# Kernel tuning notes

Hardware: AMD Instinct MI355X
Metric: run time of the kernel (lower is better)

The kernel has to match this reference:

```python
import jax, jax.numpy as jnp
import numpy as np

HEADS = 8
DK = 64            # key_size == size_per_head
NEIGHBORS = 3
KSIZE = 1 + 2 * NEIGHBORS  # 7 (rate=1)


def setup_inputs() -> dict:
    key = jax.random.key(0)
    k1, k2, k3, k4 = jax.random.split(key, 4)
    B, HW, S, D = 2, 64, 256, 512
    inputs = jax.random.normal(k1, (B, HW, S, D), dtype=jnp.float32)
    pos_bias = jax.random.normal(k2, (HEADS, S, KSIZE), dtype=jnp.float32)
    W_qkv = jax.random.normal(k3, (D, 3 * HEADS * DK), dtype=jnp.float32) * 0.02
    W_out = jax.random.normal(k4, (HEADS * DK, D), dtype=jnp.float32) * 0.02
    return {"inputs": inputs, "pos_bias": pos_bias, "W_qkv": W_qkv, "W_out": W_out}


def reference(inputs, pos_bias, W_qkv, W_out):
    B, HW, S, D = inputs.shape
    # qkv projection (no bias), split into q, k, v
    qkv = inputs @ W_qkv                                   # [B,HW,S,3*H*DK]
    q, k, v = jnp.split(qkv, 3, axis=-1)
    q = (q / jnp.sqrt(jnp.float32(DK))).reshape(B, HW, S, HEADS, DK)
    k = k.reshape(B, HW, S, HEADS, DK)
    v = v.reshape(B, HW, S, HEADS, DK)

    # zero-pad keys/values along seq (faithful to F.pad with value=0)
    pad = NEIGHBORS
    kp = jnp.pad(k, ((0, 0), (0, 0), (pad, pad), (0, 0), (0, 0)))
    vp = jnp.pad(v, ((0, 0), (0, 0), (pad, pad), (0, 0), (0, 0)))

    # sliding-window gather: window w for query i covers padded positions i..i+KSIZE-1
    idx = jnp.arange(S)[:, None] + jnp.arange(KSIZE)[None, :]  # [S,KSIZE]
    kw = kp[:, :, idx]                                         # [B,HW,S,KSIZE,H,DK]
    vw = vp[:, :, idx]                                         # [B,HW,S,KSIZE,H,DK]

    # scores over the window
    attn = jnp.einsum('bnshd,bnswhd->bnswh', q, kw)            # [B,HW,S,KSIZE,H]
    # additive positional bias: [H,S,KSIZE] -> [S,KSIZE,H] broadcast
    attn = attn + jnp.transpose(pos_bias, (1, 2, 0))[None, None]
    attn = jax.nn.softmax(attn, axis=-2)                       # softmax over window dim

    out = jnp.einsum('bnswh,bnswhd->bnshd', attn, vw)          # [B,HW,S,H,DK]
    out = out.reshape(B, HW, S, HEADS * DK)
    return out @ W_out
```

## Files before the change

kernel.cpp:

```cpp
#include <hip/hip_runtime.h>
#include <hip/hip_bf16.h>
#include <cstdint>


typedef __bf16 bf16x8 __attribute__((ext_vector_type(8)));
typedef float f32x4 __attribute__((ext_vector_type(4)));

__device__ __forceinline__ uint16_t f2bf(float f) {
    uint32_t u = __builtin_bit_cast(uint32_t, f);
    return (uint16_t)((u + 0x7fffu + ((u >> 16) & 1u)) >> 16);
}
__device__ __forceinline__ float bflo(uint32_t u) { return __builtin_bit_cast(float, u << 16); }
__device__ __forceinline__ float bfhi(uint32_t u) { return __builtin_bit_cast(float, u & 0xffff0000u); }

__device__ __forceinline__ void unpack8(uint4 v, float* f) {
    f[0] = bflo(v.x); f[1] = bfhi(v.x);
    f[2] = bflo(v.y); f[3] = bfhi(v.y);
    f[4] = bflo(v.z); f[5] = bfhi(v.z);
    f[6] = bflo(v.w); f[7] = bfhi(v.w);
}
__device__ __forceinline__ uint32_t pack2(float a, float b) {
    return (uint32_t)f2bf(a) | ((uint32_t)f2bf(b) << 16);
}

#define GLOAD_LDS16(gp, lp)                                                        \
    __builtin_amdgcn_global_load_lds((const __attribute__((address_space(1))) void*)(gp), \
                                     (__attribute__((address_space(3))) void*)(lp), 16, 0, 0)

__global__ void cvt_f32_bf16(const float* __restrict__ in, uint16_t* __restrict__ out, int n8) {
    int i = blockIdx.x * 256 + threadIdx.x;
    if (i >= n8) return;
    const float4* p = (const float4*)in + (size_t)i * 2;
    float4 a = p[0], b = p[1];
    uint4 o;
    o.x = pack2(a.x, a.y);
    o.y = pack2(a.z, a.w);
    o.z = pack2(b.x, b.y);
    o.w = pack2(b.z, b.w);
    *((uint4*)out + i) = o;
}

__global__ void transpose_cvt(const float* __restrict__ in, uint16_t* __restrict__ out,
                              int R, int C) {
    int idx = blockIdx.x * 256 + threadIdx.x;
    if (idx >= R * C) return;
    int r = idx / C;
    int c = idx - r * C;
    out[(size_t)c * R + r] = f2bf(in[idx]);
}

__global__ void frag_shuffle(const uint16_t* __restrict__ BT, uint4* __restrict__ out,
                             int N, int K) {
    int idx = blockIdx.x * 256 + threadIdx.x;
    int kt_n = K / 32;
    int total = (N / 64) * kt_n * 4 * 64;
    if (idx >= total) return;
    int lane = idx & 63;
    int nt   = (idx >> 6) & 3;
    int kt   = (idx >> 8) % kt_n;
    int g    = (idx >> 8) / kt_n;
    int row  = g * 64 + nt * 16 + (lane & 15);
    int col4 = kt * 4 + (lane >> 4);
    out[idx] = ((const uint4*)BT)[(size_t)row * (K / 8) + col4];
}

template <bool F32OUT>
__global__ __launch_bounds__(256, 4)
void gemm_bt(const uint16_t* __restrict__ A, const uint4* __restrict__ Bfrag,
             void* __restrict__ Cout, int M, int N, int K) {
    __shared__ __align__(16) uint16_t As[128 * 32];

    const int tid  = threadIdx.x;
    const int lane = tid & 63;
    const int wv   = tid >> 6;
    const int r    = lane & 15;
    const int quad = lane >> 4;
    const int m_w  = (wv & 1) << 6;
    const int n_w  = (wv >> 1) << 6;
    const long bm0 = (long)blockIdx.x * 128;
    const long bn0 = (long)blockIdx.y * 128;
    const int KT   = K / 32;

    f32x4 acc[4][4];
#pragma unroll
    for (int i = 0; i < 4; ++i)
#pragma unroll
        for (int j = 0; j < 4; ++j) acc[i][j] = (f32x4){0.f, 0.f, 0.f, 0.f};

    const int c0 = tid, c1 = tid + 256;
    const uint16_t* pA0 = A + (bm0 + (c0 >> 2)) * (long)K + (c0 & 3) * 8;
    const uint16_t* pA1 = A + (bm0 + (c1 >> 2)) * (long)K + (c1 & 3) * 8;

    const int g = (int)((bn0 + n_w) >> 6);
    const uint4* pBf = Bfrag + ((size_t)g * KT * 4) * 64 + lane;

    for (int kt = 0; kt < KT; ++kt) {
        bf16x8 bfr[4];
#pragma unroll
        for (int nt = 0; nt < 4; ++nt)
            bfr[nt] = *(const bf16x8*)&pBf[(kt * 4 + nt) * 64];

        GLOAD_LDS16(pA0 + kt * 32, &As[c0 * 8]);
        GLOAD_LDS16(pA1 + kt * 32, &As[c1 * 8]);
        __syncthreads();

        bf16x8 af[4];
#pragma unroll
        for (int mt = 0; mt < 4; ++mt)
            af[mt] = *(const bf16x8*)&As[(m_w + mt * 16 + r) * 32 + quad * 8];
#pragma unroll
        for (int mt = 0; mt < 4; ++mt)
#pragma unroll
            for (int nt = 0; nt < 4; ++nt)
                acc[mt][nt] = __builtin_amdgcn_mfma_f32_16x16x32_bf16(af[mt], bfr[nt],
                                                                      acc[mt][nt], 0, 0, 0);
        __syncthreads();
    }

#pragma unroll
    for (int mt = 0; mt < 4; ++mt) {
#pragma unroll
        for (int i = 0; i < 4; ++i) {
            long m = bm0 + m_w + mt * 16 + quad * 4 + i;
            if (F32OUT) {
                float* crow = (float*)Cout + m * (long)N + bn0 + n_w + r;
#pragma unroll
                for (int nt = 0; nt < 4; ++nt) crow[nt * 16] = acc[mt][nt][i];
            } else {
                uint16_t* crow = (uint16_t*)Cout + m * (long)N + bn0 + n_w + r;
#pragma unroll
                for (int nt = 0; nt < 4; ++nt) crow[nt * 16] = f2bf(acc[mt][nt][i]);
            }
        }
    }
}

__global__ __launch_bounds__(256, 2)
void local_attn(const uint16_t* __restrict__ qkv, const float* __restrict__ pb,
                uint16_t* __restrict__ attn) {
    __shared__ uint4 smem[4096];

    const int h  = blockIdx.x & 7;
    const int bn = blockIdx.x >> 3;
    const int s  = threadIdx.x;
    const size_t base = (size_t)bn * 256 * 1536;

#pragma unroll
    for (int it = 0; it < 16; ++it) {
        int i   = threadIdx.x + it * 256;
        int a   = i >> 11;
        int idx = i & 2047;
        int sp  = idx >> 3;
        int c8  = idx & 7;
        const uint16_t* src = qkv + base + (size_t)sp * 1536 + 512 + a * 512 + h * 64 + c8 * 8;
        smem[a * 2048 + sp * 8 + (c8 ^ (sp & 7))] = *(const uint4*)src;
    }

    const uint16_t* qrow = qkv + base + (size_t)s * 1536 + h * 64;
    uint4 qc[8];
#pragma unroll
    for (int c = 0; c < 8; ++c) qc[c] = *(const uint4*)(qrow + c * 8);

    __syncthreads();

    float sc[7];
#pragma unroll
    for (int w = 0; w < 7; ++w) sc[w] = 0.f;

#pragma unroll
    for (int c = 0; c < 8; ++c) {
        float qf[8];
        unpack8(qc[c], qf);
#pragma unroll
        for (int w = 0; w < 7; ++w) {
            int sp = s + w - 3;
            if ((unsigned)sp < 256u) {
                uint4 kc = smem[sp * 8 + (c ^ (sp & 7))];
                float kf[8];
                unpack8(kc, kf);
#pragma unroll
                for (int j = 0; j < 8; ++j) sc[w] += qf[j] * kf[j];
            }
        }
    }

    const float* pbr = pb + ((size_t)h * 256 + s) * 7;
    float mx = -1e30f;
#pragma unroll
    for (int w = 0; w < 7; ++w) {
        sc[w] = sc[w] * 0.125f + pbr[w];
        mx = fmaxf(mx, sc[w]);
    }
    float p[7], sum = 0.f;
#pragma unroll
    for (int w = 0; w < 7; ++w) {
        p[w] = __expf(sc[w] - mx);
        sum += p[w];
    }
    const float inv = 1.f / sum;
#pragma unroll
    for (int w = 0; w < 7; ++w) p[w] *= inv;

    uint4 ov[8];
#pragma unroll
    for (int c = 0; c < 8; ++c) {
        float o[8] = {0.f, 0.f, 0.f, 0.f, 0.f, 0.f, 0.f, 0.f};
#pragma unroll
        for (int w = 0; w < 7; ++w) {
            int sp = s + w - 3;
            if ((unsigned)sp < 256u) {
                uint4 vc = smem[2048 + sp * 8 + (c ^ (sp & 7))];
                float vf[8];
                unpack8(vc, vf);
#pragma unroll
                for (int j = 0; j < 8; ++j) o[j] += p[w] * vf[j];
            }
        }
        ov[c].x = pack2(o[0], o[1]);
        ov[c].y = pack2(o[2], o[3]);
        ov[c].z = pack2(o[4], o[5]);
        ov[c].w = pack2(o[6], o[7]);
    }

    uint16_t* orow = attn + ((size_t)(bn * 256 + s)) * 512 + h * 64;
#pragma unroll
    for (int c = 0; c < 8; ++c) *(uint4*)(orow + c * 8) = ov[c];
}

extern "C" void kernel_launch(void* const* d_in, const int* in_sizes, int n_in,
                              void* d_out, int out_size, void* d_ws, size_t ws_size,
                              hipStream_t stream) {
    const float* X    = (const float*)d_in[0];
    const float* pb   = (const float*)d_in[1];
    const float* Wqkv = (const float*)d_in[2];
    const float* Wout = (const float*)d_in[3];
    float* out = (float*)d_out;

    char* ws = (char*)d_ws;
    uint16_t* WqkvT  = (uint16_t*)(ws);
    uint16_t* WoutT  = (uint16_t*)(ws + 1572864);
    uint4*    BfQkv  = (uint4*)(ws + 2097152);
    uint4*    BfOut  = (uint4*)(ws + 3670016);
    uint16_t* qkvb   = (uint16_t*)(ws + 4194304);
    uint16_t* Xb     = (uint16_t*)(ws + 104857600);
    uint16_t* attnb  = Xb;

    cvt_f32_bf16<<<(32768 * 512 / 8 + 255) / 256, 256, 0, stream>>>(X, Xb, 32768 * 512 / 8);
    transpose_cvt<<<(512 * 1536 + 255) / 256, 256, 0, stream>>>(Wqkv, WqkvT, 512, 1536);
    transpose_cvt<<<(512 * 512 + 255) / 256, 256, 0, stream>>>(Wout, WoutT, 512, 512);
    frag_shuffle<<<(1536 * 512 / 8 + 255) / 256, 256, 0, stream>>>(WqkvT, BfQkv, 1536, 512);
    frag_shuffle<<<(512 * 512 / 8 + 255) / 256, 256, 0, stream>>>(WoutT, BfOut, 512, 512);

    gemm_bt<false><<<dim3(256, 12), 256, 0, stream>>>(Xb, BfQkv, qkvb, 32768, 1536, 512);
    local_attn<<<1024, 256, 0, stream>>>(qkvb, pb, attnb);
    gemm_bt<true><<<dim3(256, 4), 256, 0, stream>>>(attnb, BfOut, out, 32768, 512, 512);
}
```

Measured before the change: 272.3 us.

## Load full-K A strip into LDS once and sweep all N tiles per block

```diff
diff --git a/kernel.cpp b/kernel.cpp
--- a/kernel.cpp
+++ b/kernel.cpp
@@ -27,17 +27,31 @@
     __builtin_amdgcn_global_load_lds((const __attribute__((address_space(1))) void*)(gp), \
                                      (__attribute__((address_space(3))) void*)(lp), 16, 0, 0)
 
-__global__ void cvt_f32_bf16(const float* __restrict__ in, uint16_t* __restrict__ out, int n8) {
-    int i = blockIdx.x * 256 + threadIdx.x;
-    if (i >= n8) return;
-    const float4* p = (const float4*)in + (size_t)i * 2;
-    float4 a = p[0], b = p[1];
-    uint4 o;
-    o.x = pack2(a.x, a.y);
-    o.y = pack2(a.z, a.w);
-    o.z = pack2(b.x, b.y);
-    o.w = pack2(b.z, b.w);
-    *((uint4*)out + i) = o;
+__global__ __launch_bounds__(256)
+void cvt_shuffle(const float* __restrict__ X, uint4* __restrict__ Afrag) {
+    __shared__ uint4 lds[4096];
+    const int g64 = blockIdx.x;
+    const int tid = threadIdx.x;
+#pragma unroll
+    for (int it = 0; it < 16; ++it) {
+        int f  = it * 256 + tid;
+        int rr = f >> 6;
+        int c  = f & 63;
+        const float4* s = (const float4*)(X + ((size_t)g64 * 64 + rr) * 512 + c * 8);
+        float4 a = s[0], b = s[1];
+        uint4 o;
+        o.x = pack2(a.x, a.y);
+        o.y = pack2(a.z, a.w);
+        o.z = pack2(b.x, b.y);
+        o.w = pack2(b.z, b.w);
+        lds[rr * 64 + (c ^ (rr & 7))] = o;
+    }
+    __syncthreads();
+#pragma unroll
+    for (int it = 0; it < 16; ++it) {
+        int i = it * 256 + tid;
+        Afrag[(size_t)g64 * 4096 + i] = lds[i];
+    }
 }
 
 __global__ void transpose_cvt(const float* __restrict__ in, uint16_t* __restrict__ out,
@@ -65,71 +79,70 @@
 }
 
 template <bool F32OUT>
-__global__ __launch_bounds__(256, 4)
-void gemm_bt(const uint16_t* __restrict__ A, const uint4* __restrict__ Bfrag,
-             void* __restrict__ Cout, int M, int N, int K) {
-    __shared__ __align__(16) uint16_t As[128 * 32];
+__global__ __launch_bounds__(256, 2)
+void gemm_strip(const uint4* __restrict__ Afrag, const uint4* __restrict__ Bfrag,
+                void* __restrict__ Cout, int N) {
+    __shared__ uint4 As[4096];
 
     const int tid  = threadIdx.x;
     const int lane = tid & 63;
     const int wv   = tid >> 6;
     const int r    = lane & 15;
     const int quad = lane >> 4;
-    const int m_w  = (wv & 1) << 6;
-    const int n_w  = (wv >> 1) << 6;
-    const long bm0 = (long)blockIdx.x * 128;
-    const long bn0 = (long)blockIdx.y * 128;
-    const int KT   = K / 32;
-
-    f32x4 acc[4][4];
-#pragma unroll
-    for (int i = 0; i < 4; ++i)
-#pragma unroll
-        for (int j = 0; j < 4; ++j) acc[i][j] = (f32x4){0.f, 0.f, 0.f, 0.f};
-
-    const int c0 = tid, c1 = tid + 256;
-    const uint16_t* pA0 = A + (bm0 + (c0 >> 2)) * (long)K + (c0 & 3) * 8;
-    const uint16_t* pA1 = A + (bm0 + (c1 >> 2)) * (long)K + (c1 & 3) * 8;
-
-    const int g = (int)((bn0 + n_w) >> 6);
-    const uint4* pBf = Bfrag + ((size_t)g * KT * 4) * 64 + lane;
-
-    for (int kt = 0; kt < KT; ++kt) {
-        bf16x8 bfr[4];
-#pragma unroll
-        for (int nt = 0; nt < 4; ++nt)
-            bfr[nt] = *(const bf16x8*)&pBf[(kt * 4 + nt) * 64];
-
-        GLOAD_LDS16(pA0 + kt * 32, &As[c0 * 8]);
-        GLOAD_LDS16(pA1 + kt * 32, &As[c1 * 8]);
-        __syncthreads();
-
-        bf16x8 af[4];
-#pragma unroll
-        for (int mt = 0; mt < 4; ++mt)
-            af[mt] = *(const bf16x8*)&As[(m_w + mt * 16 + r) * 32 + quad * 8];
-#pragma unroll
-        for (int mt = 0; mt < 4; ++mt)
+    const int g64  = blockIdx.x;
+    const int NG   = N >> 6;
+
+    const uint4* src = Afrag + (size_t)g64 * 4096;
+#pragma unroll
+    for (int it = 0; it < 16; ++it) {
+        int i = it * 256 + tid;
+        GLOAD_LDS16(src + i, &As[i]);
+    }
+    __syncthreads();
+
+    const int rx = r & 7;
+
+    for (int ng = wv; ng < NG; ng += 4) {
+        f32x4 acc[4][4];
+#pragma unroll
+        for (int i = 0; i < 4; ++i)
+#pragma unroll
+            for (int j = 0; j < 4; ++j) acc[i][j] = (f32x4){0.f, 0.f, 0.f, 0.f};
+
+        const uint4* pBf = Bfrag + ((size_t)ng * 64) * 64 + lane;
+
+#pragma unroll
+        for (int kt = 0; kt < 16; ++kt) {
+            bf16x8 bfr[4];
 #pragma unroll
             for (int nt = 0; nt < 4; ++nt)
-                acc[mt][nt] = __builtin_amdgcn_mfma_f32_16x16x32_bf16(af[mt], bfr[nt],
-                                                                      acc[mt][nt], 0, 0, 0);
-        __syncthreads();
-    }
-
-#pragma unroll
-    for (int mt = 0; mt < 4; ++mt) {
-#pragma unroll
-        for (int i = 0; i < 4; ++i) {
-            long m = bm0 + m_w + mt * 16 + quad * 4 + i;
-            if (F32OUT) {
-                float* crow = (float*)Cout + m * (long)N + bn0 + n_w + r;
-#pragma unroll
-                for (int nt = 0; nt < 4; ++nt) crow[nt * 16] = acc[mt][nt][i];
-            } else {
-                uint16_t* crow = (uint16_t*)Cout + m * (long)N + bn0 + n_w + r;
-#pragma unroll
-                for (int nt = 0; nt < 4; ++nt) crow[nt * 16] = f2bf(acc[mt][nt][i]);
+                bfr[nt] = *(const bf16x8*)&pBf[(kt * 4 + nt) * 64];
+            bf16x8 af[4];
+#pragma unroll
+            for (int mt = 0; mt < 4; ++mt)
+                af[mt] = *(const bf16x8*)&As[(mt * 16 + r) * 64 + ((kt * 4 + quad) ^ rx)];
+#pragma unroll
+            for (int mt = 0; mt < 4; ++mt)
+#pragma unroll
+                for (int nt = 0; nt < 4; ++nt)
+                    acc[mt][nt] = __builtin_amdgcn_mfma_f32_16x16x32_bf16(af[mt], bfr[nt],
+                                                                          acc[mt][nt], 0, 0, 0);
+        }
+
+#pragma unroll
+        for (int mt = 0; mt < 4; ++mt) {
+#pragma unroll
+            for (int i = 0; i < 4; ++i) {
+                long m = (long)g64 * 64 + mt * 16 + quad * 4 + i;
+                if (F32OUT) {
+                    float* crow = (float*)Cout + m * (long)N + ng * 64 + r;
+#pragma unroll
+                    for (int nt = 0; nt < 4; ++nt) crow[nt * 16] = acc[mt][nt][i];
+                } else {
+                    uint16_t* crow = (uint16_t*)Cout + m * (long)N + ng * 64 + r;
+#pragma unroll
+                    for (int nt = 0; nt < 4; ++nt) crow[nt * 16] = f2bf(acc[mt][nt][i]);
+                }
             }
         }
     }
@@ -137,7 +150,7 @@
 
 __global__ __launch_bounds__(256, 2)
 void local_attn(const uint16_t* __restrict__ qkv, const float* __restrict__ pb,
-                uint16_t* __restrict__ attn) {
+                uint4* __restrict__ attnf) {
     __shared__ uint4 smem[4096];
 
     const int h  = blockIdx.x & 7;
@@ -222,9 +235,12 @@
         ov[c].w = pack2(o[6], o[7]);
     }
 
-    uint16_t* orow = attn + ((size_t)(bn * 256 + s)) * 512 + h * 64;
-#pragma unroll
-    for (int c = 0; c < 8; ++c) *(uint4*)(orow + c * 8) = ov[c];
+    const int g64 = (bn << 2) + (s >> 6);
+    const int rr  = s & 63;
+    uint4* obase = attnf + (size_t)g64 * 4096 + rr * 64;
+#pragma unroll
+    for (int cc = 0; cc < 8; ++cc)
+        obase[(h * 8 + cc) ^ (rr & 7)] = ov[cc];
 }
 
 extern "C" void kernel_launch(void* const* d_in, const int* in_sizes, int n_in,
@@ -237,21 +253,21 @@
     float* out = (float*)d_out;
 
     char* ws = (char*)d_ws;
-    uint16_t* WqkvT  = (uint16_t*)(ws);
-    uint16_t* WoutT  = (uint16_t*)(ws + 1572864);
-    uint4*    BfQkv  = (uint4*)(ws + 2097152);
-    uint4*    BfOut  = (uint4*)(ws + 3670016);
-    uint16_t* qkvb   = (uint16_t*)(ws + 4194304);
-    uint16_t* Xb     = (uint16_t*)(ws + 104857600);
-    uint16_t* attnb  = Xb;
-
-    cvt_f32_bf16<<<(32768 * 512 / 8 + 255) / 256, 256, 0, stream>>>(X, Xb, 32768 * 512 / 8);
+    uint16_t* WqkvT = (uint16_t*)(ws);
+    uint16_t* WoutT = (uint16_t*)(ws + 1572864);
+    uint4*    BfQkv = (uint4*)(ws + 2097152);
+    uint4*    BfOut = (uint4*)(ws + 3670016);
+    uint16_t* qkvb  = (uint16_t*)(ws + 4194304);
+    uint4*    Xfrag = (uint4*)(ws + 104857600);
+    uint4*    attnf = Xfrag;
+
+    cvt_shuffle<<<512, 256, 0, stream>>>(X, Xfrag);
     transpose_cvt<<<(512 * 1536 + 255) / 256, 256, 0, stream>>>(Wqkv, WqkvT, 512, 1536);
     transpose_cvt<<<(512 * 512 + 255) / 256, 256, 0, stream>>>(Wout, WoutT, 512, 512);
     frag_shuffle<<<(1536 * 512 / 8 + 255) / 256, 256, 0, stream>>>(WqkvT, BfQkv, 1536, 512);
     frag_shuffle<<<(512 * 512 / 8 + 255) / 256, 256, 0, stream>>>(WoutT, BfOut, 512, 512);
 
-    gemm_bt<false><<<dim3(256, 12), 256, 0, stream>>>(Xb, BfQkv, qkvb, 32768, 1536, 512);
-    local_attn<<<1024, 256, 0, stream>>>(qkvb, pb, attnb);
-    gemm_bt<true><<<dim3(256, 4), 256, 0, stream>>>(attnb, BfOut, out, 32768, 512, 512);
-}
+    gemm_strip<false><<<512, 256, 0, stream>>>(Xfrag, BfQkv, qkvb, 1536);
+    local_attn<<<1024, 256, 0, stream>>>(qkvb, pb, attnf);
+    gemm_strip<true><<<512, 256, 0, stream>>>(attnf, BfOut, out, 512);
+}
```

Result: slower. 376.4 us (+38.2%).
